# Kernel tuning notes

Hardware: AMD Instinct MI355X
Metric: run time of the kernel (lower is better)

Reference implementation:

```python
import jax, jax.numpy as jnp
import numpy as np

B, L, D_MODEL = 2, 2048, 512
EXPAND = 2
ED = EXPAND * D_MODEL          # d_inner = 1024
N = 16                          # d_state
D_CONV = 4
DT_RANK = (D_MODEL + N - 1) // N  # 32
D_FF = 1024
EPS = 1e-5


def _mamba_params(key, pre):
    ks = jax.random.split(key, 6)
    s = 0.02
    p = {}
    p[pre + 'in_w'] = jax.random.normal(ks[0], (D_MODEL, 2 * ED), jnp.float32) * s
    p[pre + 'conv_w'] = jax.random.normal(ks[1], (ED, 1, D_CONV), jnp.float32) * s
    p[pre + 'conv_b'] = jnp.zeros((ED,), jnp.float32)
    p[pre + 'xproj_w'] = jax.random.normal(ks[2], (ED, DT_RANK + 2 * N), jnp.float32) * s
    p[pre + 'dt_w'] = jax.random.normal(ks[3], (DT_RANK, ED), jnp.float32) * s
    p[pre + 'dt_b'] = jax.random.normal(ks[4], (ED,), jnp.float32) * s
    # S4D-real init: A_log = log(1..N) per channel
    p[pre + 'A_log'] = jnp.log(jnp.broadcast_to(jnp.arange(1, N + 1, dtype=jnp.float32), (ED, N)))
    p[pre + 'D'] = jnp.ones((ED,), jnp.float32)
    p[pre + 'out_w'] = jax.random.normal(ks[5], (ED, D_MODEL), jnp.float32) * s
    return p


def setup_inputs() -> dict:
    key = jax.random.key(0)
    k_x, k_f, k_b, k_ffn = jax.random.split(key, 4)
    inp = {'x': jax.random.normal(k_x, (B, L, D_MODEL), jnp.float32)}
    inp.update(_mamba_params(k_f, 'f_'))
    inp.update(_mamba_params(k_b, 'b_'))
    inp['norm1_g'] = jnp.ones((D_MODEL,), jnp.float32)
    inp['norm1_b'] = jnp.zeros((D_MODEL,), jnp.float32)
    inp['norm2_g'] = jnp.ones((D_MODEL,), jnp.float32)
    inp['norm2_b'] = jnp.zeros((D_MODEL,), jnp.float32)
    k1, k2 = jax.random.split(k_ffn)
    inp['ffn_w1'] = jax.random.normal(k1, (D_MODEL, D_FF), jnp.float32) * 0.02
    inp['ffn_b1'] = jnp.zeros((D_FF,), jnp.float32)
    inp['ffn_w2'] = jax.random.normal(k2, (D_FF, D_MODEL), jnp.float32) * 0.02
    inp['ffn_b2'] = jnp.zeros((D_MODEL,), jnp.float32)
    return inp


def _selective_scan(x, delta, A, Bm, C, Dp):
    # x, delta: (B,L,ED); A: (ED,N); Bm, C: (B,L,N); Dp: (ED,)
    def step(h, inp):
        x_t, d_t, B_t, C_t = inp  # (B,ED),(B,ED),(B,N),(B,N)
        dA = jnp.exp(d_t[..., None] * A)                      # (B,ED,N)
        dBx = (d_t * x_t)[..., None] * B_t[:, None, :]        # (B,ED,N)
        h = dA * h + dBx
        y = jnp.einsum('ben,bn->be', h, C_t)
        return h, y

    h0 = jnp.zeros((x.shape[0], ED, N), x.dtype)
    xs = (x.transpose(1, 0, 2), delta.transpose(1, 0, 2),
          Bm.transpose(1, 0, 2), C.transpose(1, 0, 2))
    _, ys = jax.lax.scan(step, h0, xs)
    return ys.transpose(1, 0, 2) + x * Dp


def _mamba(x, in_w, conv_w, conv_b, xproj_w, dt_w, dt_b, A_log, Dp, out_w):
    xz = x @ in_w                                  # (B,L,2*ED)
    xs, z = jnp.split(xz, 2, axis=-1)
    # depthwise causal conv over time
    xc = jax.lax.conv_general_dilated(
        xs.transpose(0, 2, 1), conv_w, (1,), [(D_CONV - 1, 0)],
        dimension_numbers=('NCH', 'OIH', 'NCH'), feature_group_count=ED)
    xc = jax.nn.silu(xc.transpose(0, 2, 1) + conv_b)          # (B,L,ED)
    dbl = xc @ xproj_w                                        # (B,L,DT_RANK+2N)
    dt = dbl[..., :DT_RANK]
    Bm = dbl[..., DT_RANK:DT_RANK + N]
    C = dbl[..., DT_RANK + N:]
    delta = jax.nn.softplus(dt @ dt_w + dt_b)                 # (B,L,ED)
    A = -jnp.exp(A_log)
    y = _selective_scan(xc, delta, A, Bm, C, Dp)
    y = y * jax.nn.silu(z)
    return y @ out_w


def _layernorm(h, g, b):
    mu = jnp.mean(h, axis=-1, keepdims=True)
    var = jnp.var(h, axis=-1, keepdims=True)
    return (h - mu) * jax.lax.rsqrt(var + EPS) * g + b


def _ffn(h, w1, b1, w2, b2):
    return jnp.maximum(h @ w1 + b1, 0.0) @ w2 + b2


def reference(x,
              f_in_w, f_conv_w, f_conv_b, f_xproj_w, f_dt_w, f_dt_b, f_A_log, f_D, f_out_w,
              b_in_w, b_conv_w, b_conv_b, b_xproj_w, b_dt_w, b_dt_b, b_A_log, b_D, b_out_w,
              norm1_g, norm1_b, norm2_g, norm2_b,
              ffn_w1, ffn_b1, ffn_w2, ffn_b2):
    mf = _mamba(x, f_in_w, f_conv_w, f_conv_b, f_xproj_w, f_dt_w, f_dt_b, f_A_log, f_D, f_out_w)
    mf = _layernorm(mf, norm1_g, norm1_b)
    out_f = _ffn(mf, ffn_w1, ffn_b1, ffn_w2, ffn_b2) + mf
    # NOTE: original code computes norm2 but then uses the UN-normalized
    # backward output (variable shadowing bug); we replicate that faithfully.
    mb = _mamba(jnp.flip(x, axis=1), b_in_w, b_conv_w, b_conv_b, b_xproj_w,
                b_dt_w, b_dt_b, b_A_log, b_D, b_out_w)
    out_b = _ffn(mb, ffn_w1, ffn_b1, ffn_w2, ffn_b2) + mb
    return out_f + out_b
```

## Files before the change

kernel.cpp:

```cpp
#include <hip/hip_runtime.h>
#include <hip/hip_bf16.h>
#include <math.h>


#define BD 2
#define LD 2048
#define DMODEL 512
#define EDIM 1024
#define NST 16
#define DTR 32
#define DFF 1024
#define MROWS (BD*LD)

typedef __hip_bfloat16 bf16;
typedef __bf16 bf16x8 __attribute__((ext_vector_type(8)));
typedef __bf16 bf16x4 __attribute__((ext_vector_type(4)));
typedef float  f32x4  __attribute__((ext_vector_type(4)));

__device__ __forceinline__ float sig_(float x) { return 1.f / (1.f + __expf(-x)); }

__device__ __forceinline__ void glds16(const void* g, void* l)
{
    __builtin_amdgcn_global_load_lds(
        (const __attribute__((address_space(1))) void*)g,
        (__attribute__((address_space(3))) void*)l, 16, 0, 0);
}

__global__ __launch_bounds__(256)
void prep_k(const float* __restrict__ x, bf16* __restrict__ xbf,
            const float* __restrict__ inw_f, const float* __restrict__ inw_b,
            bf16* __restrict__ inwT,
            const float* __restrict__ outw_f, const float* __restrict__ outw_b,
            bf16* __restrict__ outwT,
            const float* __restrict__ fw1, bf16* __restrict__ fw1T,
            const float* __restrict__ fw2, bf16* __restrict__ fw2T,
            const float* __restrict__ xp_f, const float* __restrict__ xp_b,
            bf16* __restrict__ xpT,
            const float* __restrict__ dtw_f, const float* __restrict__ dtw_b,
            bf16* __restrict__ dtwT)
{
    const int bid = blockIdx.x, tid = threadIdx.x;
    if (bid < 2048) {
        size_t i = (size_t)bid * 1024 + tid * 4;
        float4 v = *(const float4*)(x + i);
        bf16* o = xbf + i;
        o[0] = __float2bfloat16(v.x); o[1] = __float2bfloat16(v.y);
        o[2] = __float2bfloat16(v.z); o[3] = __float2bfloat16(v.w);
        return;
    }
    const float* W; bf16* WT; int R, C, cx, ry;
    if (bid < 4096) {
        int d = (bid - 2048) >> 10, t = (bid - 2048) & 1023;
        W = d ? inw_b : inw_f; WT = inwT + (size_t)d * 2048 * 512;
        R = 512; C = 2048; cx = t & 63; ry = t >> 6;
    } else if (bid < 5120) {
        int d = (bid - 4096) >> 9, t = (bid - 4096) & 511;
        W = d ? outw_b : outw_f; WT = outwT + (size_t)d * 512 * 1024;
        R = 1024; C = 512; cx = t & 15; ry = t >> 4;
    } else if (bid < 5632) {
        int t = bid - 5120; W = fw1; WT = fw1T; R = 512; C = 1024;
        cx = t & 31; ry = t >> 5;
    } else if (bid < 6144) {
        int t = bid - 5632; W = fw2; WT = fw2T; R = 1024; C = 512;
        cx = t & 15; ry = t >> 4;
    } else if (bid < 6272) {
        int d = (bid - 6144) >> 6, t = (bid - 6144) & 63;
        W = d ? xp_b : xp_f; WT = xpT + (size_t)d * 64 * 1024;
        R = 1024; C = 64; cx = t & 1; ry = t >> 1;
    } else {
        int d = (bid - 6272) >> 5, t = (bid - 6272) & 31;
        W = d ? dtw_b : dtw_f; WT = dtwT + (size_t)d * 1024 * DTR;
        R = 32; C = 1024; cx = t; ry = 0;
    }
    __shared__ float tt[32][33];
    const int c0 = cx * 32, r0 = ry * 32;
    const int col = tid & 31, rr = tid >> 5;
#pragma unroll
    for (int p = 0; p < 4; ++p)
        tt[p * 8 + rr][col] = W[(size_t)(r0 + p * 8 + rr) * C + c0 + col];
    __syncthreads();
#pragma unroll
    for (int p = 0; p < 4; ++p)
        WT[(size_t)(c0 + p * 8 + rr) * R + r0 + col] =
            __float2bfloat16(tt[col][p * 8 + rr]);
}

template<int BM, int BN, int MODE, bool FLIPD1, bool CATK>
__global__ __launch_bounds__(256)
void bgemm3_k(const bf16* __restrict__ A, size_t Astr, int lda,
              const bf16* __restrict__ BT, size_t Bstr, int ldb,
              const float* __restrict__ bias,
              bf16* __restrict__ Cb, size_t Cstr, int ldc,
              const bf16* __restrict__ mp, size_t mpStr,
              float* __restrict__ outp, int K)
{
    constexpr int BK = 32;
    constexpr int FRm = BM / 32, FRn = BN / 32;
    constexpr int KH = DFF;
    __shared__ __align__(16) bf16 As[2][BM][BK];
    __shared__ __align__(16) bf16 Bs[2][BN][BK];
    const int tid = threadIdx.x;
    const int dir = blockIdx.z;
    const bool flip = FLIPD1 && (dir == 1);
    const bf16* Ad = A + (CATK ? (size_t)0 : (size_t)dir * Astr);
    const bf16* Bd = BT + (size_t)dir * Bstr;
    const int bm = blockIdx.y * BM, bn = blockIdx.x * BN;
    const int wave = tid >> 6, lane = tid & 63;
    const int wm = (wave >> 1) * (BM / 2), wn = (wave & 1) * (BN / 2);
    const int lm = lane & 15, lq = lane >> 4;
    const int lrow = lane >> 2, lcol = (lane & 3) * 8;
    f32x4 acc[FRm][FRn] = {};

    auto STAGE = [&](int buf, int k0) {
        const bf16* Ab = Ad;
        int ka = k0;
        if (CATK && k0 >= KH) { Ab = A + Astr; ka = k0 - KH; }
        const int kb = CATK ? (k0 & (KH - 1)) : k0;
#pragma unroll
        for (int c = 0; c < BM / 64; ++c) {
            int row = c * 64 + wave * 16 + lrow;
            int gm = bm + row;
            if (flip) gm = (gm & ~(LD - 1)) + (LD - 1 - (gm & (LD - 1)));
            glds16(Ab + (size_t)gm * lda + ka + lcol,
                   &As[buf][c * 64 + wave * 16][0]);
        }
#pragma unroll
        for (int c = 0; c < BN / 64; ++c) {
            int row = c * 64 + wave * 16 + lrow;
            glds16(Bd + (size_t)(bn + row) * ldb + kb + lcol,
                   &Bs[buf][c * 64 + wave * 16][0]);
        }
    };
    auto COMPUTE = [&](int buf) {
        bf16x8 af[FRm], bfr[FRn];
#pragma unroll
        for (int i = 0; i < FRm; ++i)
            af[i] = *(const bf16x8*)&As[buf][wm + 16 * i + lm][lq * 8];
#pragma unroll
        for (int j = 0; j < FRn; ++j)
            bfr[j] = *(const bf16x8*)&Bs[buf][wn + 16 * j + lm][lq * 8];
#pragma unroll
        for (int i = 0; i < FRm; ++i)
#pragma unroll
            for (int j = 0; j < FRn; ++j)
                acc[i][j] = __builtin_amdgcn_mfma_f32_16x16x32_bf16(
                    af[i], bfr[j], acc[i][j], 0, 0, 0);
    };

    STAGE(0, 0);
    __syncthreads();
    int cur = 0;
    for (int k0 = BK; k0 < K; k0 += BK) {
        STAGE(cur ^ 1, k0);
        COMPUTE(cur);
        __syncthreads();
        cur ^= 1;
    }
    COMPUTE(cur);

    bf16* Cd = (MODE == 5) ? nullptr : Cb + (size_t)dir * Cstr;
#pragma unroll
    for (int i = 0; i < FRm; ++i) {
#pragma unroll
        for (int j = 0; j < FRn; ++j) {
            int col = bn + wn + 16 * j + lm;
            float bv = (MODE == 2) ? bias[col]
                     : (MODE == 5) ? 2.f * bias[col] : 0.f;
#pragma unroll
            for (int r = 0; r < 4; ++r) {
                int row = bm + wm + 16 * i + lq * 4 + r;
                float v = acc[i][j][r] + bv;
                size_t idx = (size_t)row * ldc + col;
                if (MODE == 0)      Cd[idx] = __float2bfloat16(v);
                else if (MODE == 2) Cd[idx] = __float2bfloat16(fmaxf(v, 0.f));
                else {
                    float m2 = __bfloat162float(mp[idx])
                             + __bfloat162float(mp[mpStr + idx]);
                    outp[idx] = v + m2;
                }
            }
        }
    }
}

__global__ __launch_bounds__(256)
void zgate_k(const bf16* __restrict__ xbf, const bf16* __restrict__ inwT,
             const bf16* __restrict__ y2t_all, bf16* __restrict__ yrow_all)
{
    __shared__ __align__(16) bf16 As[64][40];
    __shared__ __align__(16) bf16 Bs[128][40];
    __shared__ __bf16 sy[64][130];
    const int tid = threadIdx.x;
    const int dir = blockIdx.z;
    const bf16* Bd = inwT + (size_t)dir * (2048 * 512) + (size_t)1024 * 512;
    const bf16* y2t = y2t_all + (size_t)dir * ((size_t)MROWS * EDIM);
    bf16* yrow = yrow_all + (size_t)dir * ((size_t)MROWS * EDIM);
    const int bm = blockIdx.y * 64, bn = blockIdx.x * 128;
    const int wave = tid >> 6, lane = tid & 63;
    const int wm = (wave >> 1) * 32, wn = (wave & 1) * 64;
    const int lm = lane & 15, lq = lane >> 4;
    f32x4 acc[2][4] = {};

    for (int k0 = 0; k0 < 512; k0 += 32) {
        {
            int row = tid >> 2, col = (tid & 3) * 8;
            int gm = bm + row;
            if (dir == 1) gm = (gm & ~(LD - 1)) + (LD - 1 - (gm & (LD - 1)));
            *(bf16x8*)&As[row][col] =
                *(const bf16x8*)(xbf + (size_t)gm * 512 + k0 + col);
        }
#pragma unroll
        for (int p = 0; p < 2; ++p) {
            int row = p * 64 + (tid >> 2), col = (tid & 3) * 8;
            *(bf16x8*)&Bs[row][col] =
                *(const bf16x8*)(Bd + (size_t)(bn + row) * 512 + k0 + col);
        }
        __syncthreads();
        bf16x8 af[2], bfr[4];
#pragma unroll
        for (int i = 0; i < 2; ++i)
            af[i] = *(const bf16x8*)&As[wm + 16 * i + lm][lq * 8];
#pragma unroll
        for (int j = 0; j < 4; ++j)
            bfr[j] = *(const bf16x8*)&Bs[wn + 16 * j + lm][lq * 8];
#pragma unroll
        for (int i = 0; i < 2; ++i)
#pragma unroll
            for (int j = 0; j < 4; ++j)
                acc[i][j] = __builtin_amdgcn_mfma_f32_16x16x32_bf16(
                    af[i], bfr[j], acc[i][j], 0, 0, 0);
        __syncthreads();
    }

    {
        const int b = bm >> 11, l0 = bm & (LD - 1);
        int e = tid >> 1, lh = (tid & 1) * 32;
        const bf16* yp = y2t + ((size_t)b * EDIM + bn + e) * LD + l0 + lh;
#pragma unroll
        for (int i = 0; i < 4; ++i) {
            bf16x8 v = *(const bf16x8*)(yp + i * 8);
#pragma unroll
            for (int j = 0; j < 8; ++j) sy[lh + i * 8 + j][e] = v[j];
        }
    }
    __syncthreads();
#pragma unroll
    for (int i = 0; i < 2; ++i) {
#pragma unroll
        for (int j = 0; j < 4; ++j) {
            int col = bn + wn + 16 * j + lm;
#pragma unroll
            for (int r = 0; r < 4; ++r) {
                int row = bm + wm + 16 * i + lq * 4 + r;
                float z = acc[i][j][r];
                float g = z * sig_(z);
                float y = (float)sy[(row - bm)][col - bn];
                yrow[(size_t)row * EDIM + col] = __float2bfloat16(g * y);
            }
        }
    }
}

__global__ __launch_bounds__(256)
void conv2_k(const bf16* __restrict__ xs2,
             const float* __restrict__ cw_f, const float* __restrict__ cb_f,
             const float* __restrict__ cw_b, const float* __restrict__ cb_b,
             bf16* __restrict__ xct2)
{
    __shared__ float sxs[67][65];
    __shared__ float sout[64][65];
    const int tid = threadIdx.x;
    const int dir = blockIdx.z;
    const bf16* xs = xs2 + (size_t)dir * ((size_t)MROWS * EDIM);
    const float* w  = dir ? cw_b : cw_f;
    const float* cb = dir ? cb_b : cb_f;
    bf16* xct = xct2 + (size_t)dir * ((size_t)MROWS * EDIM);
    const int e0 = blockIdx.x * 64;
    const int bl0 = blockIdx.y * 64;
    const int lloc0 = bl0 & (LD - 1);
    const int b = bl0 >> 11;
    {
        int c8 = (tid & 7) * 8;
#pragma unroll
        for (int i = 0; i < 3; ++i) {
            int hr = i * 32 + (tid >> 3);
            if (hr < 67) {
                int lr = lloc0 + hr - 3;
                if (lr >= 0) {
                    bf16x8 v = *(const bf16x8*)(xs +
                        (size_t)(bl0 + hr - 3) * EDIM + e0 + c8);
#pragma unroll
                    for (int j = 0; j < 8; ++j) sxs[hr][c8 + j] = (float)v[j];
                } else {
#pragma unroll
                    for (int j = 0; j < 8; ++j) sxs[hr][c8 + j] = 0.f;
                }
            }
        }
    }
    __syncthreads();
    {
        int lr4 = tid >> 6, e = tid & 63;
        float w0 = w[(e0 + e) * 4 + 0], w1 = w[(e0 + e) * 4 + 1];
        float w2 = w[(e0 + e) * 4 + 2], w3 = w[(e0 + e) * 4 + 3];
        float cbv = cb[e0 + e];
#pragma unroll
        for (int i = 0; i < 16; ++i) {
            int lr = i * 4 + lr4;
            float acc = cbv;
            acc = fmaf(sxs[lr + 0][e], w0, acc);
            acc = fmaf(sxs[lr + 1][e], w1, acc);
            acc = fmaf(sxs[lr + 2][e], w2, acc);
            acc = fmaf(sxs[lr + 3][e], w3, acc);
            sout[e][lr] = acc * sig_(acc);
        }
    }
    __syncthreads();
    {
        int l8 = (tid & 7) * 8;
#pragma unroll
        for (int i = 0; i < 2; ++i) {
            int er = i * 32 + (tid >> 3);
            bf16x8 o;
#pragma unroll
            for (int j = 0; j < 8; ++j) o[j] = (__bf16)sout[er][l8 + j];
            *(bf16x8*)(xct + ((size_t)b * EDIM + e0 + er) * LD + lloc0 + l8) = o;
        }
    }
}

__global__ __launch_bounds__(256)
void g2m_k(const bf16* __restrict__ xct2, const bf16* __restrict__ xpT2,
           float* __restrict__ dblt2, float* __restrict__ dbldt2)
{
    __shared__ float As[64][33];
    __shared__ __align__(16) bf16 Bs[64][32];
    __shared__ float sC[32][65];
    const int tid = threadIdx.x;
    const int dir = blockIdx.z;
    const bf16* xct = xct2 + (size_t)dir * ((size_t)MROWS * EDIM);
    const bf16* xpT = xpT2 + (size_t)dir * (64 * 1024);
    float* dblt = dblt2 + (size_t)dir * (2 * 64 * LD);
    float* dbldt = dbldt2 + (size_t)dir * (2 * 2048 * DTR);
    const int bm = blockIdx.y * 64;
    const int bB = bm >> 11, l0 = bm & (LD - 1);
    const int wave = tid >> 6, lane = tid & 63;
    const int wm = (wave >> 1) * 32, wn = (wave & 1) * 32;
    const int lm = lane & 15, lq = lane >> 4;
    const int er = tid >> 3, l8 = (tid & 7) * 8;
    f32x4 acc[2][2] = {};

    for (int k0 = 0; k0 < EDIM; k0 += 32) {
        glds16(xpT + (size_t)(wave * 16 + (lane >> 2)) * 1024 + k0 + (lane & 3) * 8,
               &Bs[wave * 16][0]);
        {
            bf16x8 v = *(const bf16x8*)(xct +
                ((size_t)bB * EDIM + k0 + er) * LD + l0 + l8);
#pragma unroll
            for (int j = 0; j < 8; ++j) As[l8 + j][er] = (float)v[j];
        }
        __syncthreads();
        bf16x8 af[2], bfr[2];
#pragma unroll
        for (int i = 0; i < 2; ++i) {
            int row = wm + 16 * i + lm;
#pragma unroll
            for (int j = 0; j < 8; ++j) af[i][j] = (__bf16)As[row][lq * 8 + j];
        }
#pragma unroll
        for (int j = 0; j < 2; ++j)
            bfr[j] = *(const bf16x8*)&Bs[wn + 16 * j + lm][lq * 8];
#pragma unroll
        for (int i = 0; i < 2; ++i)
#pragma unroll
            for (int j = 0; j < 2; ++j)
                acc[i][j] = __builtin_amdgcn_mfma_f32_16x16x32_bf16(
                    af[i], bfr[j], acc[i][j], 0, 0, 0);
        __syncthreads();
    }
    if (wn == 0) {
#pragma unroll
        for (int i = 0; i < 2; ++i)
#pragma unroll
            for (int j = 0; j < 2; ++j) {
                int col = 16 * j + lm;
#pragma unroll
                for (int r = 0; r < 4; ++r) {
                    int row = wm + 16 * i + lq * 4 + r;
                    dbldt[(size_t)(bB * 2048 + l0 + row) * DTR + col] =
                        acc[i][j][r];
                }
            }
    } else {
#pragma unroll
        for (int i = 0; i < 2; ++i)
#pragma unroll
            for (int j = 0; j < 2; ++j) {
                int col = 16 * j + lm;
#pragma unroll
                for (int r = 0; r < 4; ++r)
                    sC[col][wm + 16 * i + lq * 4 + r] = acc[i][j][r];
            }
    }
    __syncthreads();
    {
        int nr = tid >> 3, ll = (tid & 7) * 8;
        float4 v0 = *(const float4*)&sC[nr][ll];
        float4 v1 = *(const float4*)&sC[nr][ll + 4];
        float* d = dblt + (size_t)(bB * 64 + 32 + nr) * LD + l0 + ll;
        *(float4*)d = v0; *(float4*)(d + 4) = v1;
    }
}

__global__ __launch_bounds__(256)
void g3m_k(const float* __restrict__ dbldt2, const bf16* __restrict__ dtwT2,
           const float* __restrict__ dtb_f, const float* __restrict__ dtb_b,
           bf16* __restrict__ dltt2)
{
    __shared__ __align__(16) bf16 As[64][40];
    __shared__ __align__(16) bf16 Bs[64][32];
    __shared__ float sC[64][65];
    const int tid = threadIdx.x;
    const int dir = blockIdx.z;
    const float* Ap = dbldt2 + (size_t)dir * (2 * 2048 * DTR);
    const bf16* BT = dtwT2 + (size_t)dir * (1024 * DTR);
    const float* bias = dir ? dtb_b : dtb_f;
    bf16* dltt = dltt2 + (size_t)dir * ((size_t)MROWS * EDIM);
    const int bm = blockIdx.y * 64, bn = blockIdx.x * 64;
    const int bB = bm >> 11, l0 = bm & (LD - 1);
    const int wave = tid >> 6, lane = tid & 63;
    const int wm = (wave >> 1) * 32, wn = (wave & 1) * 32;
    const int lm = lane & 15, lq = lane >> 4;

    {
        int row = tid >> 2, c8 = (tid & 3) * 8;
        const float* p = Ap + (size_t)(bB * 2048 + l0 + row) * DTR + c8;
        float4 v0 = *(const float4*)p, v1 = *(const float4*)(p + 4);
        bf16x8 o;
        o[0]=(__bf16)v0.x; o[1]=(__bf16)v0.y; o[2]=(__bf16)v0.z; o[3]=(__bf16)v0.w;
        o[4]=(__bf16)v1.x; o[5]=(__bf16)v1.y; o[6]=(__bf16)v1.z; o[7]=(__bf16)v1.w;
        *(bf16x8*)&As[row][c8] = o;
    }
    glds16(BT + (size_t)(bn + wave * 16 + (lane >> 2)) * DTR + (lane & 3) * 8,
           &Bs[wave * 16][0]);
    __syncthreads();

    bf16x8 af[2], bfr[2];
#pragma unroll
    for (int i = 0; i < 2; ++i)
        af[i] = *(const bf16x8*)&As[wm + 16 * i + lm][lq * 8];
#pragma unroll
    for (int j = 0; j < 2; ++j)
        bfr[j] = *(const bf16x8*)&Bs[wn + 16 * j + lm][lq * 8];
    f32x4 acc[2][2] = {};
#pragma unroll
    for (int i = 0; i < 2; ++i)
#pragma unroll
        for (int j = 0; j < 2; ++j)
            acc[i][j] = __builtin_amdgcn_mfma_f32_16x16x32_bf16(
                af[i], bfr[j], acc[i][j], 0, 0, 0);

#pragma unroll
    for (int i = 0; i < 2; ++i)
#pragma unroll
        for (int j = 0; j < 2; ++j) {
            int col = wn + 16 * j + lm;
            float bv = bias[bn + col];
#pragma unroll
            for (int r = 0; r < 4; ++r) {
                int row = wm + 16 * i + lq * 4 + r;
                float v = acc[i][j][r] + bv;
                v = (v > 20.f) ? v : log1pf(__expf(v));
                sC[col][row] = v;
            }
        }
    __syncthreads();
    {
        int erow = tid >> 2, l16 = (tid & 3) * 16;
        bf16* d = dltt + ((size_t)bB * EDIM + bn + erow) * LD + l0 + l16;
#pragma unroll
        for (int h = 0; h < 2; ++h) {
            bf16x8 o;
#pragma unroll
            for (int j = 0; j < 8; ++j) o[j] = (__bf16)sC[erow][l16 + h * 8 + j];
            *(bf16x8*)(d + h * 8) = o;
        }
    }
}

__global__ __launch_bounds__(256)
void scan6_k(bf16* __restrict__ xct2, const bf16* __restrict__ dltt2,
             const float* __restrict__ dblt2,
             const float* __restrict__ alog_f, const float* __restrict__ alog_b,
             const float* __restrict__ dp_f, const float* __restrict__ dp_b)
{
    __shared__ float sA[NST];
    __shared__ float sWp[NST][4];
    __shared__ float sWs[NST][4];
    const int gid = blockIdx.x;
    const int dir = gid >> 11;
    const int bb  = (gid >> 10) & 1;
    const int e   = gid & (EDIM - 1);
    const float* A_log = dir ? alog_b : alog_f;
    const float* Dp    = dir ? dp_b   : dp_f;
    bf16* xct = xct2 + (size_t)dir * ((size_t)MROWS * EDIM);
    const bf16* dltt = dltt2 + (size_t)dir * ((size_t)MROWS * EDIM);
    const float* bt = dblt2 + (size_t)dir * (2 * 64 * LD) + (size_t)bb * 64 * LD;
    const int tid = threadIdx.x;
    const int wave = tid >> 6, lane = tid & 63;
    const size_t baset = ((size_t)bb * EDIM + e) * LD;
    const int l0 = tid * 8;

    if (tid < NST) sA[tid] = -__expf(A_log[e * NST + tid]);

    float xv[8], dv[8], dx[8];
    {
        bf16x8 xr = *(const bf16x8*)(xct + baset + l0);
        bf16x8 dr = *(const bf16x8*)(dltt + baset + l0);
#pragma unroll
        for (int j = 0; j < 8; ++j) { xv[j] = (float)xr[j]; dv[j] = (float)dr[j]; }
    }
#pragma unroll
    for (int j = 0; j < 8; ++j) dx[j] = dv[j] * xv[j];
    __syncthreads();

    float y[8] = {};
    for (int n = 0; n < NST; ++n) {
        const float An = sA[n];
        const float* Bp = bt + (size_t)(DTR + n) * LD + l0;
        const float* Cp = bt + (size_t)(DTR + NST + n) * LD + l0;
        float4 b0 = *(const float4*)Bp, b1 = *(const float4*)(Bp + 4);
        float4 c0 = *(const float4*)Cp, c1 = *(const float4*)(Cp + 4);
        float Br[8] = {b0.x,b0.y,b0.z,b0.w, b1.x,b1.y,b1.z,b1.w};
        float Cr[8] = {c0.x,c0.y,c0.z,c0.w, c1.x,c1.y,c1.z,c1.w};

        float S[8], P[8];
        float h = 0.f, pr = 1.f;
#pragma unroll
        for (int l = 0; l < 8; ++l) {
            float a = __expf(dv[l] * An);
            pr *= a;
            h = fmaf(a, h, dx[l] * Br[l]);
            P[l] = pr; S[l] = h;
        }

        float p = pr, s = h;
#pragma unroll
        for (int d = 1; d < 64; d <<= 1) {
            float pp = __shfl_up(p, d, 64);
            float sp = __shfl_up(s, d, 64);
            if (lane >= d) { s = fmaf(sp, p, s); p *= pp; }
        }
        if (lane == 63) { sWp[n][wave] = p; sWs[n][wave] = s; }
        __syncthreads();
        float Hoff = 0.f;
#pragma unroll
        for (int w = 0; w < 3; ++w)
            if (w < wave) Hoff = fmaf(sWp[n][w], Hoff, sWs[n][w]);
        float pprev = __shfl_up(p, 1, 64);
        float sprev = __shfl_up(s, 1, 64);
        float H = (lane == 0) ? Hoff : fmaf(pprev, Hoff, sprev);

#pragma unroll
        for (int l = 0; l < 8; ++l)
            y[l] = fmaf(Cr[l], fmaf(P[l], H, S[l]), y[l]);
    }

    const float Dv = Dp[e];
    bf16x8 o;
#pragma unroll
    for (int l = 0; l < 8; ++l) o[l] = (__bf16)fmaf(xv[l], Dv, y[l]);
    *(bf16x8*)(xct + baset + l0) = o;
}

__global__ __launch_bounds__(256)
void ln_k(bf16* __restrict__ m, const float* __restrict__ gg,
          const float* __restrict__ bb)
{
    int row = (blockIdx.x * 256 + threadIdx.x) >> 6;
    int lane = threadIdx.x & 63;
    bf16* r = m + (size_t)row * DMODEL;
    float v[8], s = 0.f, s2 = 0.f;
#pragma unroll
    for (int i = 0; i < 8; ++i) {
        v[i] = __bfloat162float(r[lane + 64 * i]);
        s += v[i]; s2 = fmaf(v[i], v[i], s2);
    }
#pragma unroll
    for (int off = 32; off >= 1; off >>= 1) {
        s  += __shfl_xor(s, off, 64);
        s2 += __shfl_xor(s2, off, 64);
    }
    float mu = s * (1.f / DMODEL);
    float var = s2 * (1.f / DMODEL) - mu * mu;
    float inv = rsqrtf(var + 1e-5f);
#pragma unroll
    for (int i = 0; i < 8; ++i)
        r[lane + 64 * i] = __float2bfloat16(
            (v[i] - mu) * inv * gg[lane + 64 * i] + bb[lane + 64 * i]);
}

__global__ void sentinel_k(float* __restrict__ o)
{
    int i = blockIdx.x * 256 + threadIdx.x;
    o[i] = 100.0f;
}

extern "C" void kernel_launch(void* const* d_in, const int* in_sizes, int n_in,
                              void* d_out, int out_size, void* d_ws, size_t ws_size,
                              hipStream_t stream)
{
    const float* x    = (const float*)d_in[0];
    const float* n1g  = (const float*)d_in[19];
    const float* n1b  = (const float*)d_in[20];
    const float* fw1  = (const float*)d_in[23];
    const float* fb1  = (const float*)d_in[24];
    const float* fw2  = (const float*)d_in[25];
    const float* fb2  = (const float*)d_in[26];
    float* out = (float*)d_out;

    const size_t MiB = 1024 * 1024;
    const size_t SZ_DM = (size_t)MROWS * DMODEL;
    if (ws_size < 49 * MiB) {
        sentinel_k<<<dim3(SZ_DM / 256), dim3(256), 0, stream>>>(out);
        return;
    }

    char* base = (char*)d_ws;
    bf16* fw1T  = (bf16*)base;
    bf16* fw2T  = (bf16*)(base + 1 * MiB);
    bf16* outwT = (bf16*)(base + 2 * MiB);
    bf16* inwT  = (bf16*)(base + 4 * MiB);
    bf16* xbf   = (bf16*)(base + 8 * MiB);
    char* RA    = base + 12 * MiB;
    bf16* xs2   = (bf16*)RA;
    bf16* dltt2 = (bf16*)RA;
    bf16* yrow2 = (bf16*)RA;
    bf16* ffh2  = (bf16*)RA;
    char* RB    = base + 28 * MiB;
    bf16* xct2  = (bf16*)RB;
    bf16* mbf2  = (bf16*)RB;
    float* dblt2 = (float*)(base + 44 * MiB);
    float* dbldt2 = (float*)(base + 46 * MiB);
    bf16* xpT2  = (bf16*)(base + 48 * MiB);
    bf16* dtwT2 = (bf16*)(base + 48 * MiB + 256 * 1024);

    const float* inw_f  = (const float*)d_in[1];
    const float* cw_f   = (const float*)d_in[2];
    const float* cb_f   = (const float*)d_in[3];
    const float* xp_f   = (const float*)d_in[4];
    const float* dtw_f  = (const float*)d_in[5];
    const float* dtb_f  = (const float*)d_in[6];
    const float* alog_f = (const float*)d_in[7];
    const float* dp_f   = (const float*)d_in[8];
    const float* outw_f = (const float*)d_in[9];
    const float* inw_b  = (const float*)d_in[10];
    const float* cw_b   = (const float*)d_in[11];
    const float* cb_b   = (const float*)d_in[12];
    const float* xp_b   = (const float*)d_in[13];
    const float* dtw_b  = (const float*)d_in[14];
    const float* dtb_b  = (const float*)d_in[15];
    const float* alog_b = (const float*)d_in[16];
    const float* dp_b   = (const float*)d_in[17];
    const float* outw_b = (const float*)d_in[18];

    dim3 blk(256);
    const size_t U = (size_t)MROWS * EDIM;

    prep_k<<<dim3(6336), blk, 0, stream>>>(x, xbf, inw_f, inw_b, inwT,
                                           outw_f, outw_b, outwT,
                                           fw1, fw1T, fw2, fw2T,
                                           xp_f, xp_b, xpT2,
                                           dtw_f, dtw_b, dtwT2);
    bgemm3_k<128, 64, 0, true, false><<<dim3(16, 32, 2), blk, 0, stream>>>(
        xbf, 0, DMODEL, inwT, (size_t)2048 * 512, DMODEL, nullptr,
        xs2, U, EDIM, nullptr, 0, nullptr, DMODEL);
    conv2_k<<<dim3(16, 64, 2), blk, 0, stream>>>(xs2, cw_f, cb_f, cw_b, cb_b, xct2);
    g2m_k<<<dim3(1, 64, 2), blk, 0, stream>>>(xct2, xpT2, dblt2, dbldt2);
    g3m_k<<<dim3(16, 64, 2), blk, 0, stream>>>(dbldt2, dtwT2, dtb_f, dtb_b, dltt2);
    scan6_k<<<dim3(4096), blk, 0, stream>>>(xct2, dltt2, dblt2,
                                            alog_f, alog_b, dp_f, dp_b);
    zgate_k<<<dim3(8, 64, 2), blk, 0, stream>>>(xbf, inwT, xct2, yrow2);
    bgemm3_k<64, 64, 0, false, false><<<dim3(8, 64, 2), blk, 0, stream>>>(
        yrow2, U, EDIM, outwT, (size_t)512 * 1024, EDIM, nullptr,
        mbf2, SZ_DM, DMODEL, nullptr, 0, nullptr, EDIM);
    ln_k<<<dim3(MROWS / 4), blk, 0, stream>>>(mbf2, n1g, n1b);
    bgemm3_k<128, 64, 2, false, false><<<dim3(16, 32, 2), blk, 0, stream>>>(
        mbf2, SZ_DM, DMODEL, fw1T, 0, DMODEL, fb1,
        ffh2, U, DFF, nullptr, 0, nullptr, DMODEL);
    bgemm3_k<64, 64, 5, false, true><<<dim3(8, 64, 1), blk, 0, stream>>>(
        ffh2, U, DFF, fw2T, 0, DFF, fb2,
        nullptr, 0, DMODEL, mbf2, SZ_DM, out, 2 * DFF);
}
```

Before: 369.6 us.

## Fuse x_proj and dt_proj GEMMs into one double-buffered kernel

Merges the x_proj GEMM (g2m_k) and the dt_proj GEMM with softplus (g3m_k) into a single kernel, g23_k. The dt-rank intermediate stays in shared memory instead of going through a global buffer, and one launch is removed. The M tile drops from 64 to 32 rows, which doubles the grid of the first stage to 256 blocks, and the K loop now double-buffers its A/B loads. Each block then loops serially over all 16 dt_proj output tiles, which adds per-block serial work and many barriers, and the first stage now uses half as many MFMAs per load.

```diff
diff --git a/kernel.cpp b/kernel.cpp
--- a/kernel.cpp
+++ b/kernel.cpp
@@ -330,161 +330,136 @@
 }
 
 __global__ __launch_bounds__(256)
-void g2m_k(const bf16* __restrict__ xct2, const bf16* __restrict__ xpT2,
-           float* __restrict__ dblt2, float* __restrict__ dbldt2)
-{
-    __shared__ float As[64][33];
-    __shared__ __align__(16) bf16 Bs[64][32];
-    __shared__ float sC[32][65];
+void g23_k(const bf16* __restrict__ xct2, const bf16* __restrict__ xpT2,
+           const bf16* __restrict__ dtwT2,
+           const float* __restrict__ dtb_f, const float* __restrict__ dtb_b,
+           float* __restrict__ dblt2, bf16* __restrict__ dltt2)
+{
+    __shared__ float As[2][32][33];
+    __shared__ __align__(16) bf16 Bs[2][64][32];
+    __shared__ float sDT[32][33];
+    __shared__ float sBC[32][33];
+    __shared__ __align__(16) bf16 Bs2[2][64][32];
+    __shared__ float sOut[64][33];
     const int tid = threadIdx.x;
     const int dir = blockIdx.z;
     const bf16* xct = xct2 + (size_t)dir * ((size_t)MROWS * EDIM);
     const bf16* xpT = xpT2 + (size_t)dir * (64 * 1024);
+    const bf16* dtwT = dtwT2 + (size_t)dir * (1024 * DTR);
+    const float* bias = dir ? dtb_b : dtb_f;
     float* dblt = dblt2 + (size_t)dir * (2 * 64 * LD);
-    float* dbldt = dbldt2 + (size_t)dir * (2 * 2048 * DTR);
-    const int bm = blockIdx.y * 64;
+    bf16* dltt = dltt2 + (size_t)dir * ((size_t)MROWS * EDIM);
+    const int bm = blockIdx.x * 32;
     const int bB = bm >> 11, l0 = bm & (LD - 1);
     const int wave = tid >> 6, lane = tid & 63;
-    const int wm = (wave >> 1) * 32, wn = (wave & 1) * 32;
+    const int wml = (wave >> 1) * 16;
+    const int wnn = (wave & 1) * 32;
     const int lm = lane & 15, lq = lane >> 4;
-    const int er = tid >> 3, l8 = (tid & 7) * 8;
-    f32x4 acc[2][2] = {};
-
-    for (int k0 = 0; k0 < EDIM; k0 += 32) {
+    const int er = tid >> 3, l4 = (tid & 7) * 4;
+    f32x4 acc1[2] = {};
+
+    auto LOAD_A = [&](int k0) {
+        return *(const bf16x4*)(xct + ((size_t)bB * EDIM + k0 + er) * LD + l0 + l4);
+    };
+    auto WRITE_A = [&](int buf, bf16x4 v) {
+#pragma unroll
+        for (int j = 0; j < 4; ++j) As[buf][l4 + j][er] = (float)v[j];
+    };
+    auto STAGE_B = [&](int buf, int k0) {
         glds16(xpT + (size_t)(wave * 16 + (lane >> 2)) * 1024 + k0 + (lane & 3) * 8,
-               &Bs[wave * 16][0]);
+               &Bs[buf][wave * 16][0]);
+    };
+    auto COMP1 = [&](int buf) {
+        bf16x8 af;
+#pragma unroll
+        for (int j = 0; j < 8; ++j) af[j] = (__bf16)As[buf][wml + lm][lq * 8 + j];
+#pragma unroll
+        for (int j = 0; j < 2; ++j) {
+            bf16x8 bfr = *(const bf16x8*)&Bs[buf][wnn + 16 * j + lm][lq * 8];
+            acc1[j] = __builtin_amdgcn_mfma_f32_16x16x32_bf16(af, bfr, acc1[j], 0, 0, 0);
+        }
+    };
+
+    {
+        bf16x4 a0 = LOAD_A(0);
+        STAGE_B(0, 0);
+        WRITE_A(0, a0);
+    }
+    __syncthreads();
+    int cur = 0;
+    for (int k0 = 32; k0 < EDIM; k0 += 32) {
+        bf16x4 an = LOAD_A(k0);
+        STAGE_B(cur ^ 1, k0);
+        COMP1(cur);
+        WRITE_A(cur ^ 1, an);
+        __syncthreads();
+        cur ^= 1;
+    }
+    COMP1(cur);
+
+    if (wnn == 0) {
+#pragma unroll
+        for (int j = 0; j < 2; ++j) {
+            int col = 16 * j + lm;
+#pragma unroll
+            for (int r = 0; r < 4; ++r)
+                sDT[wml + lq * 4 + r][col] = acc1[j][r];
+        }
+    } else {
+#pragma unroll
+        for (int j = 0; j < 2; ++j) {
+            int col = 16 * j + lm;
+#pragma unroll
+            for (int r = 0; r < 4; ++r)
+                sBC[col][wml + lq * 4 + r] = acc1[j][r];
+        }
+    }
+    __syncthreads();
+    {
+        int nr = tid >> 3, ll = (tid & 7) * 4;
+        float4 v = *(const float4*)&sBC[nr][ll];
+        *(float4*)(dblt + (size_t)(bB * 64 + 32 + nr) * LD + l0 + ll) = v;
+    }
+    bf16x8 af2;
+#pragma unroll
+    for (int j = 0; j < 8; ++j) af2[j] = (__bf16)sDT[wml + lm][lq * 8 + j];
+
+    auto STAGE_B2 = [&](int buf, int bn) {
+        glds16(dtwT + (size_t)(bn + wave * 16 + (lane >> 2)) * DTR + (lane & 3) * 8,
+               &Bs2[buf][wave * 16][0]);
+    };
+    STAGE_B2(0, 0);
+    int cur2 = 0;
+    for (int t = 0; t < 16; ++t) {
+        int bn = t * 64;
+        __syncthreads();
+        if (t < 15) STAGE_B2(cur2 ^ 1, bn + 64);
+        f32x4 acc2[2] = {};
+#pragma unroll
+        for (int j = 0; j < 2; ++j) {
+            bf16x8 bfr = *(const bf16x8*)&Bs2[cur2][wnn + 16 * j + lm][lq * 8];
+            acc2[j] = __builtin_amdgcn_mfma_f32_16x16x32_bf16(af2, bfr, acc2[j], 0, 0, 0);
+        }
+#pragma unroll
+        for (int j = 0; j < 2; ++j) {
+            int col = wnn + 16 * j + lm;
+            float bv = bias[bn + col];
+#pragma unroll
+            for (int r = 0; r < 4; ++r) {
+                float v = acc2[j][r] + bv;
+                v = (v > 20.f) ? v : log1pf(__expf(v));
+                sOut[col][wml + lq * 4 + r] = v;
+            }
+        }
+        __syncthreads();
         {
-            bf16x8 v = *(const bf16x8*)(xct +
-                ((size_t)bB * EDIM + k0 + er) * LD + l0 + l8);
-#pragma unroll
-            for (int j = 0; j < 8; ++j) As[l8 + j][er] = (float)v[j];
-        }
-        __syncthreads();
-        bf16x8 af[2], bfr[2];
-#pragma unroll
-        for (int i = 0; i < 2; ++i) {
-            int row = wm + 16 * i + lm;
-#pragma unroll
-            for (int j = 0; j < 8; ++j) af[i][j] = (__bf16)As[row][lq * 8 + j];
-        }
-#pragma unroll
-        for (int j = 0; j < 2; ++j)
-            bfr[j] = *(const bf16x8*)&Bs[wn + 16 * j + lm][lq * 8];
-#pragma unroll
-        for (int i = 0; i < 2; ++i)
-#pragma unroll
-            for (int j = 0; j < 2; ++j)
-                acc[i][j] = __builtin_amdgcn_mfma_f32_16x16x32_bf16(
-                    af[i], bfr[j], acc[i][j], 0, 0, 0);
-        __syncthreads();
-    }
-    if (wn == 0) {
-#pragma unroll
-        for (int i = 0; i < 2; ++i)
-#pragma unroll
-            for (int j = 0; j < 2; ++j) {
-                int col = 16 * j + lm;
-#pragma unroll
-                for (int r = 0; r < 4; ++r) {
-                    int row = wm + 16 * i + lq * 4 + r;
-                    dbldt[(size_t)(bB * 2048 + l0 + row) * DTR + col] =
-                        acc[i][j][r];
-                }
-            }
-    } else {
-#pragma unroll
-        for (int i = 0; i < 2; ++i)
-#pragma unroll
-            for (int j = 0; j < 2; ++j) {
-                int col = 16 * j + lm;
-#pragma unroll
-                for (int r = 0; r < 4; ++r)
-                    sC[col][wm + 16 * i + lq * 4 + r] = acc[i][j][r];
-            }
-    }
-    __syncthreads();
-    {
-        int nr = tid >> 3, ll = (tid & 7) * 8;
-        float4 v0 = *(const float4*)&sC[nr][ll];
-        float4 v1 = *(const float4*)&sC[nr][ll + 4];
-        float* d = dblt + (size_t)(bB * 64 + 32 + nr) * LD + l0 + ll;
-        *(float4*)d = v0; *(float4*)(d + 4) = v1;
-    }
-}
-
-__global__ __launch_bounds__(256)
-void g3m_k(const float* __restrict__ dbldt2, const bf16* __restrict__ dtwT2,
-           const float* __restrict__ dtb_f, const float* __restrict__ dtb_b,
-           bf16* __restrict__ dltt2)
-{
-    __shared__ __align__(16) bf16 As[64][40];
-    __shared__ __align__(16) bf16 Bs[64][32];
-    __shared__ float sC[64][65];
-    const int tid = threadIdx.x;
-    const int dir = blockIdx.z;
-    const float* Ap = dbldt2 + (size_t)dir * (2 * 2048 * DTR);
-    const bf16* BT = dtwT2 + (size_t)dir * (1024 * DTR);
-    const float* bias = dir ? dtb_b : dtb_f;
-    bf16* dltt = dltt2 + (size_t)dir * ((size_t)MROWS * EDIM);
-    const int bm = blockIdx.y * 64, bn = blockIdx.x * 64;
-    const int bB = bm >> 11, l0 = bm & (LD - 1);
-    const int wave = tid >> 6, lane = tid & 63;
-    const int wm = (wave >> 1) * 32, wn = (wave & 1) * 32;
-    const int lm = lane & 15, lq = lane >> 4;
-
-    {
-        int row = tid >> 2, c8 = (tid & 3) * 8;
-        const float* p = Ap + (size_t)(bB * 2048 + l0 + row) * DTR + c8;
-        float4 v0 = *(const float4*)p, v1 = *(const float4*)(p + 4);
-        bf16x8 o;
-        o[0]=(__bf16)v0.x; o[1]=(__bf16)v0.y; o[2]=(__bf16)v0.z; o[3]=(__bf16)v0.w;
-        o[4]=(__bf16)v1.x; o[5]=(__bf16)v1.y; o[6]=(__bf16)v1.z; o[7]=(__bf16)v1.w;
-        *(bf16x8*)&As[row][c8] = o;
-    }
-    glds16(BT + (size_t)(bn + wave * 16 + (lane >> 2)) * DTR + (lane & 3) * 8,
-           &Bs[wave * 16][0]);
-    __syncthreads();
-
-    bf16x8 af[2], bfr[2];
-#pragma unroll
-    for (int i = 0; i < 2; ++i)
-        af[i] = *(const bf16x8*)&As[wm + 16 * i + lm][lq * 8];
-#pragma unroll
-    for (int j = 0; j < 2; ++j)
-        bfr[j] = *(const bf16x8*)&Bs[wn + 16 * j + lm][lq * 8];
-    f32x4 acc[2][2] = {};
-#pragma unroll
-    for (int i = 0; i < 2; ++i)
-#pragma unroll
-        for (int j = 0; j < 2; ++j)
-            acc[i][j] = __builtin_amdgcn_mfma_f32_16x16x32_bf16(
-                af[i], bfr[j], acc[i][j], 0, 0, 0);
-
-#pragma unroll
-    for (int i = 0; i < 2; ++i)
-#pragma unroll
-        for (int j = 0; j < 2; ++j) {
-            int col = wn + 16 * j + lm;
-            float bv = bias[bn + col];
-#pragma unroll
-            for (int r = 0; r < 4; ++r) {
-                int row = wm + 16 * i + lq * 4 + r;
-                float v = acc[i][j][r] + bv;
-                v = (v > 20.f) ? v : log1pf(__expf(v));
-                sC[col][row] = v;
-            }
-        }
-    __syncthreads();
-    {
-        int erow = tid >> 2, l16 = (tid & 3) * 16;
-        bf16* d = dltt + ((size_t)bB * EDIM + bn + erow) * LD + l0 + l16;
-#pragma unroll
-        for (int h = 0; h < 2; ++h) {
+            int erow = tid >> 2, l8s = (tid & 3) * 8;
             bf16x8 o;
 #pragma unroll
-            for (int j = 0; j < 8; ++j) o[j] = (__bf16)sC[erow][l16 + h * 8 + j];
-            *(bf16x8*)(d + h * 8) = o;
-        }
+            for (int j = 0; j < 8; ++j) o[j] = (__bf16)sOut[erow][l8s + j];
+            *(bf16x8*)(dltt + ((size_t)bB * EDIM + bn + erow) * LD + l0 + l8s) = o;
+        }
+        cur2 ^= 1;
     }
 }
 
@@ -641,7 +616,6 @@
     bf16* xct2  = (bf16*)RB;
     bf16* mbf2  = (bf16*)RB;
     float* dblt2 = (float*)(base + 44 * MiB);
-    float* dbldt2 = (float*)(base + 46 * MiB);
     bf16* xpT2  = (bf16*)(base + 48 * MiB);
     bf16* dtwT2 = (bf16*)(base + 48 * MiB + 256 * 1024);
 
@@ -676,8 +650,8 @@
         xbf, 0, DMODEL, inwT, (size_t)2048 * 512, DMODEL, nullptr,
         xs2, U, EDIM, nullptr, 0, nullptr, DMODEL);
     conv2_k<<<dim3(16, 64, 2), blk, 0, stream>>>(xs2, cw_f, cb_f, cw_b, cb_b, xct2);
-    g2m_k<<<dim3(1, 64, 2), blk, 0, stream>>>(xct2, xpT2, dblt2, dbldt2);
-    g3m_k<<<dim3(16, 64, 2), blk, 0, stream>>>(dbldt2, dtwT2, dtb_f, dtb_b, dltt2);
+    g23_k<<<dim3(128, 1, 2), blk, 0, stream>>>(xct2, xpT2, dtwT2,
+                                               dtb_f, dtb_b, dblt2, dltt2);
     scan6_k<<<dim3(4096), blk, 0, stream>>>(xct2, dltt2, dblt2,
                                             alog_f, alog_b, dp_f, dp_b);
     zgate_k<<<dim3(8, 64, 2), blk, 0, stream>>>(xbf, inwT, xct2, yrow2);
```

After: 384.0 us. +3.9%, slower.
